# Kernel optimization log

Hardware: AMD Instinct MI355X
Metric: run time of the kernel (lower is better)

Reference implementation:

```python
import jax, jax.numpy as jnp
import numpy as np

N, E, G = 50000, 800000, 256
F_IN, H, C = 128, 64, 10
BN_EPS = 1e-5
N_CONV = 3


def _bn(x, g, b):
    # training-mode BatchNorm1d: biased batch statistics over dim 0
    m = jnp.mean(x, axis=0)
    v = jnp.mean((x - m) ** 2, axis=0)
    return g * (x - m) * jax.lax.rsqrt(v + BN_EPS) + b


def setup_inputs() -> dict:
    key = jax.random.key(0)
    ks = jax.random.split(key, 16)
    w = lambda k, s: jax.random.normal(k, s, jnp.float32) * 0.1
    inp = {
        "x": jax.random.normal(ks[0], (N, F_IN), jnp.float32),
        "edge_index": jax.random.randint(ks[1], (2, E), 0, N, jnp.int32),
        "batch": jnp.sort(jax.random.randint(ks[2], (N,), 0, G, jnp.int32)),
        # bn_feat
        "bn_feat_g": jnp.ones((F_IN,), jnp.float32),
        "bn_feat_b": jnp.full((F_IN,), 1e-4, jnp.float32),
        # conv_feat: GCNConv(gfn=True) == plain Linear
        "w_feat": w(ks[3], (F_IN, H)),
        "b_feat": jnp.zeros((H,), jnp.float32),
        # 3 GIN layers, params stacked on leading axis
        "gin_w1": w(ks[4], (N_CONV, H, H)),
        "gin_b1": jnp.zeros((N_CONV, H), jnp.float32),
        "gin_bn_g": jnp.ones((N_CONV, H), jnp.float32),
        "gin_bn_b": jnp.full((N_CONV, H), 1e-4, jnp.float32),
        "gin_w2": w(ks[5], (N_CONV, H, H)),
        "gin_b2": jnp.zeros((N_CONV, H), jnp.float32),
        # FC head: one bn+linear (num_fc_layers=2), bn_hidden, lin_class
        "bn_fc_g": jnp.ones((H,), jnp.float32),
        "bn_fc_b": jnp.full((H,), 1e-4, jnp.float32),
        "lin_w": w(ks[6], (H, H)),
        "lin_b": jnp.zeros((H,), jnp.float32),
        "bn_h_g": jnp.ones((H,), jnp.float32),
        "bn_h_b": jnp.full((H,), 1e-4, jnp.float32),
        "cls_w": w(ks[7], (H, C)),
        "cls_b": jnp.zeros((C,), jnp.float32),
    }
    return inp


def reference(x, edge_index, batch, bn_feat_g, bn_feat_b, w_feat, b_feat,
              gin_w1, gin_b1, gin_bn_g, gin_bn_b, gin_w2, gin_b2,
              bn_fc_g, bn_fc_b, lin_w, lin_b, bn_h_g, bn_h_b, cls_w, cls_b):
    src, dst = edge_index[0], edge_index[1]
    h = _bn(x, bn_feat_g, bn_feat_b)
    h = jax.nn.relu(h @ w_feat + b_feat)  # GCNConv(gfn=True): linear only
    for i in range(N_CONV):
        # GIN: (1+eps)*x + sum_{j in N(i)} x_j, eps = 0
        agg = jax.ops.segment_sum(h[src], dst, num_segments=N)
        z = h + agg
        z = jax.nn.relu(_bn(z @ gin_w1[i] + gin_b1[i], gin_bn_g[i], gin_bn_b[i]))
        h = jax.nn.relu(z @ gin_w2[i] + gin_b2[i])
    hg = jax.ops.segment_sum(h, batch, num_segments=G)  # global_add_pool
    hg = jax.nn.relu(_bn(hg, bn_fc_g, bn_fc_b) @ lin_w + lin_b)
    hg = _bn(hg, bn_h_g, bn_h_b)
    return hg @ cls_w + cls_b  # [G, C]
```

## Files before the change

kernel.cpp:

```cpp
#include <hip/hip_runtime.h>
#include <hip/hip_bf16.h>

#define NN 50000
#define EE 800000
#define GG 256
#define FF 128
#define HH 64
#define CC 10
#define BN_EPS 1e-5f
#define NB_SCAN ((NN + 255) / 256)

__device__ __forceinline__ float lane_bcast(float v, int srcLane) {
    union { float f; int i; } u; u.f = v;
    u.i = __builtin_amdgcn_readlane(u.i, srcLane);
    return u.f;
}

__global__ __launch_bounds__(256) void colstats128(const float* __restrict__ x,
                                                   float* __restrict__ sums, int n) {
    const int ROWS = (NN + 255) >> 8;
    int col = threadIdx.x & 127;
    int rh  = threadIdx.x >> 7;
    int r0  = blockIdx.x * ROWS;
    int r1  = min(n, r0 + ROWS);
    float s = 0.f, sq = 0.f;
    for (int r = r0 + rh; r < r1; r += 2) {
        float v = x[(size_t)r * FF + col];
        s += v; sq += v * v;
    }
    __shared__ float ls[256], lq[256];
    ls[threadIdx.x] = s; lq[threadIdx.x] = sq;
    __syncthreads();
    if (threadIdx.x < 128) {
        atomicAdd(&sums[col], ls[threadIdx.x] + ls[threadIdx.x + 128]);
        atomicAdd(&sums[128 + col], lq[threadIdx.x] + lq[threadIdx.x + 128]);
    }
}

__global__ void fold_feat(const float* __restrict__ sums, const float* __restrict__ g,
                          const float* __restrict__ b, const float* __restrict__ W,
                          const float* __restrict__ bias_in, float* __restrict__ Wf,
                          float* __restrict__ bf, float invn) {
    __shared__ float a[FF], c[FF];
    int j = threadIdx.x;
    float m = sums[j] * invn;
    float v = sums[FF + j] * invn - m * m;
    float aj = g[j] * rsqrtf(v + BN_EPS);
    a[j] = aj;
    c[j] = fmaf(-aj, m, b[j]);
    __syncthreads();
    for (int idx = j; idx < FF * HH; idx += FF) {
        int jj = idx >> 6;
        Wf[idx] = a[jj] * W[idx];
    }
    if (j < HH) {
        float acc = bias_in[j];
        for (int jj = 0; jj < FF; jj++) acc = fmaf(c[jj], W[jj * HH + j], acc);
        bf[j] = acc;
    }
}

__global__ __launch_bounds__(256) void gemm_feat(const float* __restrict__ x,
                                                 const float* __restrict__ Wf,
                                                 const float* __restrict__ bf,
                                                 float* __restrict__ h, int n) {
    int lane = threadIdx.x & 63;
    int wid  = threadIdx.x >> 6;
    float w[FF];
#pragma unroll
    for (int j = 0; j < FF; j++) w[j] = Wf[j * HH + lane];
    float bv = bf[lane];
    int wstride = gridDim.x * 4;
    for (int r = blockIdx.x * 4 + wid; r < n; r += wstride) {
        float xa = x[(size_t)r * FF + lane];
        float xb = x[(size_t)r * FF + 64 + lane];
        float a0 = bv, a1 = 0.f, a2 = 0.f, a3 = 0.f;
#pragma unroll
        for (int j = 0; j < 64; j += 4) {
            a0 = fmaf(lane_bcast(xa, j),     w[j],     a0);
            a1 = fmaf(lane_bcast(xa, j + 1), w[j + 1], a1);
            a2 = fmaf(lane_bcast(xa, j + 2), w[j + 2], a2);
            a3 = fmaf(lane_bcast(xa, j + 3), w[j + 3], a3);
        }
#pragma unroll
        for (int j = 0; j < 64; j += 4) {
            a0 = fmaf(lane_bcast(xb, j),     w[64 + j],     a0);
            a1 = fmaf(lane_bcast(xb, j + 1), w[64 + j + 1], a1);
            a2 = fmaf(lane_bcast(xb, j + 2), w[64 + j + 2], a2);
            a3 = fmaf(lane_bcast(xb, j + 3), w[64 + j + 3], a3);
        }
        h[(size_t)r * HH + lane] = fmaxf((a0 + a1) + (a2 + a3), 0.f);
    }
}

__global__ void hist_kernel(const int* __restrict__ dst, int* __restrict__ cnt, int e) {
    int i = blockIdx.x * blockDim.x + threadIdx.x;
    if (i < e) atomicAdd(&cnt[dst[i]], 1);
}

__global__ __launch_bounds__(256) void tile_sums(const int* __restrict__ cnt,
                                                 int* __restrict__ bsum, int n) {
    __shared__ int red[256];
    int i = blockIdx.x * 256 + threadIdx.x;
    red[threadIdx.x] = (i < n) ? cnt[i] : 0;
    __syncthreads();
    for (int off = 128; off > 0; off >>= 1) {
        if (threadIdx.x < off) red[threadIdx.x] += red[threadIdx.x + off];
        __syncthreads();
    }
    if (threadIdx.x == 0) bsum[blockIdx.x] = red[0];
}

__global__ __launch_bounds__(256) void scan_bsums(int* __restrict__ bsum, int nb) {
    __shared__ int s[256];
    int t = threadIdx.x;
    int v = (t < nb) ? bsum[t] : 0;
    s[t] = v;
    __syncthreads();
    for (int off = 1; off < 256; off <<= 1) {
        int x = (t >= off) ? s[t - off] : 0;
        __syncthreads();
        s[t] += x;
        __syncthreads();
    }
    if (t < nb) bsum[t] = s[t] - v;
}

__global__ __launch_bounds__(256) void scan_tiles_write(const int* __restrict__ cnt,
                                                        const int* __restrict__ bscan,
                                                        int* __restrict__ rowptr, int n) {
    __shared__ int s[256];
    int b = blockIdx.x, t = threadIdx.x;
    int i = b * 256 + t;
    int v = (i < n) ? cnt[i] : 0;
    s[t] = v;
    __syncthreads();
    for (int off = 1; off < 256; off <<= 1) {
        int x = (t >= off) ? s[t - off] : 0;
        __syncthreads();
        s[t] += x;
        __syncthreads();
    }
    if (i < n) rowptr[i] = bscan[b] + s[t] - v;
    if (b == 0 && t == 0) rowptr[n] = EE;
}

__global__ void fill_csr(const int* __restrict__ src, const int* __restrict__ dst,
                         const int* __restrict__ rowptr, int* __restrict__ cursor,
                         int* __restrict__ csr, int e) {
    int i = blockIdx.x * blockDim.x + threadIdx.x;
    if (i < e) {
        int d = dst[i];
        int slot = rowptr[d] + atomicAdd(&cursor[d], 1);
        csr[slot] = src[i];
    }
}

__global__ __launch_bounds__(256) void aggregate(const float* __restrict__ hin,
                                                 const int* __restrict__ rowptr,
                                                 const int* __restrict__ csr,
                                                 float* __restrict__ z, int n) {
    int lane  = threadIdx.x & 63;
    int wid   = threadIdx.x >> 6;
    int qcol  = (lane & 15) << 2;
    int eslot = lane >> 4;
    int wstride = gridDim.x * 4;
    for (int node = blockIdx.x * 4 + wid; node < n; node += wstride) {
        int lo = rowptr[node], hi = rowptr[node + 1];
        float ax = 0.f, ay = 0.f, az = 0.f, aw = 0.f;
        int base = lo;
        for (; base + 8 <= hi; base += 8) {
            int s0 = csr[base + eslot];
            int s1 = csr[base + 4 + eslot];
            const float4 v0 = *reinterpret_cast<const float4*>(&hin[(size_t)s0 * HH + qcol]);
            const float4 v1 = *reinterpret_cast<const float4*>(&hin[(size_t)s1 * HH + qcol]);
            ax += v0.x + v1.x; ay += v0.y + v1.y;
            az += v0.z + v1.z; aw += v0.w + v1.w;
        }
        if (base + 4 <= hi) {
            int s0 = csr[base + eslot];
            const float4 v0 = *reinterpret_cast<const float4*>(&hin[(size_t)s0 * HH + qcol]);
            ax += v0.x; ay += v0.y; az += v0.z; aw += v0.w;
            base += 4;
        }
        int rem = hi - base;
        if (eslot < rem) {
            int s0 = csr[base + eslot];
            const float4 v0 = *reinterpret_cast<const float4*>(&hin[(size_t)s0 * HH + qcol]);
            ax += v0.x; ay += v0.y; az += v0.z; aw += v0.w;
        }
        ax += __shfl_xor(ax, 16); ay += __shfl_xor(ay, 16);
        az += __shfl_xor(az, 16); aw += __shfl_xor(aw, 16);
        ax += __shfl_xor(ax, 32); ay += __shfl_xor(ay, 32);
        az += __shfl_xor(az, 32); aw += __shfl_xor(aw, 32);
        if (eslot == 0) {
            const float4 self = *reinterpret_cast<const float4*>(&hin[(size_t)node * HH + qcol]);
            float4 o;
            o.x = ax + self.x; o.y = ay + self.y;
            o.z = az + self.z; o.w = aw + self.w;
            *reinterpret_cast<float4*>(&z[(size_t)node * HH + qcol]) = o;
        }
    }
}

__global__ __launch_bounds__(256) void gin_lin1(float* __restrict__ zy,
                                                const float* __restrict__ W,
                                                const float* __restrict__ bias,
                                                float* __restrict__ stats, int n) {
    int lane = threadIdx.x & 63;
    int wid  = threadIdx.x >> 6;
    float w[HH];
#pragma unroll
    for (int j = 0; j < HH; j++) w[j] = W[j * HH + lane];
    float bv = bias[lane];
    float s = 0.f, sq = 0.f;
    int wstride = gridDim.x * 4;
    for (int r = blockIdx.x * 4 + wid; r < n; r += wstride) {
        float zv = zy[(size_t)r * HH + lane];
        float a0 = bv, a1 = 0.f;
#pragma unroll
        for (int j = 0; j < HH; j += 2) {
            a0 = fmaf(lane_bcast(zv, j),     w[j],     a0);
            a1 = fmaf(lane_bcast(zv, j + 1), w[j + 1], a1);
        }
        float acc = a0 + a1;
        zy[(size_t)r * HH + lane] = acc;
        s += acc; sq += acc * acc;
    }
    atomicAdd(&stats[lane], s);
    atomicAdd(&stats[HH + lane], sq);
}

__global__ void bn_params(const float* __restrict__ stats, const float* __restrict__ g,
                          const float* __restrict__ b, float* __restrict__ ac,
                          float invn, int cols) {
    int k = threadIdx.x;
    if (k < cols) {
        float m = stats[k] * invn;
        float v = stats[cols + k] * invn - m * m;
        float a = g[k] * rsqrtf(v + BN_EPS);
        ac[k] = a;
        ac[cols + k] = fmaf(-a, m, b[k]);
    }
}

__global__ __launch_bounds__(256) void gin_lin2(float* __restrict__ yh,
                                                const float* __restrict__ ac,
                                                const float* __restrict__ W2,
                                                const float* __restrict__ b2, int n) {
    int lane = threadIdx.x & 63;
    int wid  = threadIdx.x >> 6;
    float w[HH];
#pragma unroll
    for (int j = 0; j < HH; j++) w[j] = W2[j * HH + lane];
    float a = ac[lane], c = ac[HH + lane];
    float bv = b2[lane];
    int wstride = gridDim.x * 4;
    for (int r = blockIdx.x * 4 + wid; r < n; r += wstride) {
        float yv = yh[(size_t)r * HH + lane];
        float zv = fmaxf(fmaf(a, yv, c), 0.f);
        float a0 = bv, a1 = 0.f;
#pragma unroll
        for (int j = 0; j < HH; j += 2) {
            a0 = fmaf(lane_bcast(zv, j),     w[j],     a0);
            a1 = fmaf(lane_bcast(zv, j + 1), w[j + 1], a1);
        }
        yh[(size_t)r * HH + lane] = fmaxf(a0 + a1, 0.f);
    }
}

__global__ __launch_bounds__(64) void pool_kernel(const float* __restrict__ h,
                                                  const int* __restrict__ batch,
                                                  float* __restrict__ hg, int n) {
    int g = blockIdx.x;
    int lo = 0, hi = n;
    while (lo < hi) { int mid = (lo + hi) >> 1; if (batch[mid] < g) lo = mid + 1; else hi = mid; }
    int start = lo;
    lo = start; hi = n;
    while (lo < hi) { int mid = (lo + hi) >> 1; if (batch[mid] < g + 1) lo = mid + 1; else hi = mid; }
    int end = lo;
    int lane = threadIdx.x;
    float acc = 0.f;
    for (int r = start; r < end; r++) acc += h[(size_t)r * HH + lane];
    hg[g * HH + lane] = acc;
}

__global__ __launch_bounds__(256) void head1(const float* __restrict__ hg,
                                             const float* __restrict__ g,
                                             const float* __restrict__ b,
                                             const float* __restrict__ lw,
                                             const float* __restrict__ lb,
                                             float* __restrict__ hh) {
    __shared__ float Wt[HH * HH];
    __shared__ float s1[256], s2[256];
    __shared__ float aa[HH], cc[HH];
    int t = threadIdx.x;
    for (int i = t; i < HH * HH; i += 256) {
        int j = i >> 6, k = i & 63;
        Wt[k * HH + j] = lw[i];
    }
    int col = t & 63, q = t >> 6;
    float s = 0.f, sq = 0.f;
    for (int r = q; r < GG; r += 4) { float v = hg[r * HH + col]; s += v; sq += v * v; }
    s1[t] = s; s2[t] = sq;
    __syncthreads();
    if (t < HH) {
        float S = s1[t] + s1[t + 64] + s1[t + 128] + s1[t + 192];
        float Q = s2[t] + s2[t + 64] + s2[t + 128] + s2[t + 192];
        float m = S * (1.f / GG), v = Q * (1.f / GG) - m * m;
        float a = g[t] * rsqrtf(v + BN_EPS);
        aa[t] = a; cc[t] = fmaf(-a, m, b[t]);
    }
    __syncthreads();
    float rv[HH];
#pragma unroll
    for (int j = 0; j < HH; j++) rv[j] = fmaf(aa[j], hg[t * HH + j], cc[j]);
#pragma unroll 4
    for (int k = 0; k < HH; k++) {
        float acc = lb[k];
#pragma unroll
        for (int j = 0; j < HH; j++) acc = fmaf(rv[j], Wt[k * HH + j], acc);
        hh[t * HH + k] = fmaxf(acc, 0.f);
    }
}

__global__ __launch_bounds__(256) void head2(const float* __restrict__ hh,
                                             const float* __restrict__ g,
                                             const float* __restrict__ b,
                                             const float* __restrict__ cw,
                                             const float* __restrict__ cb,
                                             float* __restrict__ out) {
    __shared__ float s1[256], s2[256];
    __shared__ float aa[HH], cc[HH];
    __shared__ float Wc[HH * CC];
    __shared__ float cbs[CC];
    int t = threadIdx.x;
    for (int i = t; i < HH * CC; i += 256) Wc[i] = cw[i];
    if (t < CC) cbs[t] = cb[t];
    int col = t & 63, q = t >> 6;
    float s = 0.f, sq = 0.f;
    for (int r = q; r < GG; r += 4) { float v = hh[r * HH + col]; s += v; sq += v * v; }
    s1[t] = s; s2[t] = sq;
    __syncthreads();
    if (t < HH) {
        float S = s1[t] + s1[t + 64] + s1[t + 128] + s1[t + 192];
        float Q = s2[t] + s2[t + 64] + s2[t + 128] + s2[t + 192];
        float m = S * (1.f / GG), v = Q * (1.f / GG) - m * m;
        float a = g[t] * rsqrtf(v + BN_EPS);
        aa[t] = a; cc[t] = fmaf(-a, m, b[t]);
    }
    __syncthreads();
    float acc[CC];
#pragma unroll
    for (int c2 = 0; c2 < CC; c2++) acc[c2] = cbs[c2];
#pragma unroll
    for (int j = 0; j < HH; j++) {
        float v = fmaf(aa[j], hh[t * HH + j], cc[j]);
#pragma unroll
        for (int c2 = 0; c2 < CC; c2++) acc[c2] = fmaf(v, Wc[j * CC + c2], acc[c2]);
    }
#pragma unroll
    for (int c2 = 0; c2 < CC; c2++) out[t * CC + c2] = acc[c2];
}

extern "C" void kernel_launch(void* const* d_in, const int* in_sizes, int n_in,
                              void* d_out, int out_size, void* d_ws, size_t ws_size,
                              hipStream_t stream) {
    const float* x        = (const float*)d_in[0];
    const int*   ei       = (const int*)d_in[1];
    const int*   srcp     = ei;
    const int*   dstp     = ei + EE;
    const int*   batchp   = (const int*)d_in[2];
    const float* bnf_g    = (const float*)d_in[3];
    const float* bnf_b    = (const float*)d_in[4];
    const float* w_feat   = (const float*)d_in[5];
    const float* b_feat   = (const float*)d_in[6];
    const float* gin_w1   = (const float*)d_in[7];
    const float* gin_b1   = (const float*)d_in[8];
    const float* gin_bn_g = (const float*)d_in[9];
    const float* gin_bn_b = (const float*)d_in[10];
    const float* gin_w2   = (const float*)d_in[11];
    const float* gin_b2   = (const float*)d_in[12];
    const float* bn_fc_g  = (const float*)d_in[13];
    const float* bn_fc_b  = (const float*)d_in[14];
    const float* lin_w    = (const float*)d_in[15];
    const float* lin_b    = (const float*)d_in[16];
    const float* bn_h_g   = (const float*)d_in[17];
    const float* bn_h_b   = (const float*)d_in[18];
    const float* cls_w    = (const float*)d_in[19];
    const float* cls_b    = (const float*)d_in[20];
    float* out = (float*)d_out;

    float* ws   = (float*)d_ws;
    float* bufA = ws;
    float* bufB = bufA + (size_t)NN * HH;
    float* Wf   = bufB + (size_t)NN * HH;
    float* bff  = Wf + FF * HH;
    float* stats= bff + HH;
    float* ac   = stats + 2 * FF;
    float* hh   = ac + 2 * HH;
    float* hg   = hh + GG * HH;
    int* rowptr = (int*)(hg + GG * HH);
    int* cnt    = rowptr + (NN + 1);
    int* bsum   = cnt + NN;
    int* csr    = bsum + NB_SCAN;

    hipMemsetAsync(stats, 0, 2 * FF * sizeof(float), stream);
    colstats128<<<256, 256, 0, stream>>>(x, stats, NN);
    fold_feat<<<1, 128, 0, stream>>>(stats, bnf_g, bnf_b, w_feat, b_feat, Wf, bff, 1.0f / NN);
    gemm_feat<<<512, 256, 0, stream>>>(x, Wf, bff, bufA, NN);

    hipMemsetAsync(cnt, 0, NN * sizeof(int), stream);
    hist_kernel<<<(EE + 255) / 256, 256, 0, stream>>>(dstp, cnt, EE);
    tile_sums<<<NB_SCAN, 256, 0, stream>>>(cnt, bsum, NN);
    scan_bsums<<<1, 256, 0, stream>>>(bsum, NB_SCAN);
    scan_tiles_write<<<NB_SCAN, 256, 0, stream>>>(cnt, bsum, rowptr, NN);
    hipMemsetAsync(cnt, 0, NN * sizeof(int), stream);
    fill_csr<<<(EE + 255) / 256, 256, 0, stream>>>(srcp, dstp, rowptr, cnt, csr, EE);

    float* hin = bufA;
    float* hout = bufB;
    for (int i = 0; i < 3; i++) {
        aggregate<<<2048, 256, 0, stream>>>(hin, rowptr, csr, hout, NN);
        hipMemsetAsync(stats, 0, 2 * HH * sizeof(float), stream);
        gin_lin1<<<512, 256, 0, stream>>>(hout, gin_w1 + i * HH * HH, gin_b1 + i * HH, stats, NN);
        bn_params<<<1, 64, 0, stream>>>(stats, gin_bn_g + i * HH, gin_bn_b + i * HH, ac, 1.0f / NN, HH);
        gin_lin2<<<512, 256, 0, stream>>>(hout, ac, gin_w2 + i * HH * HH, gin_b2 + i * HH, NN);
        float* tmp = hin; hin = hout; hout = tmp;
    }

    pool_kernel<<<GG, 64, 0, stream>>>(hin, batchp, hg, NN);
    head1<<<1, 256, 0, stream>>>(hg, bn_fc_g, bn_fc_b, lin_w, lin_b, hh);
    head2<<<1, 256, 0, stream>>>(hh, bn_h_g, bn_h_b, cls_w, cls_b, out);
}
```

Baseline: 733.3 us.

## Stage GIN linear rows in shared memory tiles and widen pooling blocks

The GIN linear kernels now load 64-row tiles into shared memory with float4 loads and read the row operand from LDS as float4 broadcasts, replacing the per-element readlane broadcasts. BN-apply+ReLU is applied during the staging load in gin_lin2. One block per tile is launched, which also brings __syncthreads overhead and extra LDS traffic. Pooling uses 256 threads per graph with a shared-memory reduction instead of one 64-thread serial loop.

```diff
diff --git a/kernel.cpp b/kernel.cpp
--- a/kernel.cpp
+++ b/kernel.cpp
@@ -9,6 +9,8 @@
 #define CC 10
 #define BN_EPS 1e-5f
 #define NB_SCAN ((NN + 255) / 256)
+#define TROWS 64
+#define NTILES ((NN + TROWS - 1) / TROWS)
 
 __device__ __forceinline__ float lane_bcast(float v, int srcLane) {
     union { float f; int i; } u; u.f = v;
@@ -207,6 +209,7 @@
                                                 const float* __restrict__ W,
                                                 const float* __restrict__ bias,
                                                 float* __restrict__ stats, int n) {
+    __shared__ float zt[TROWS][HH];
     int lane = threadIdx.x & 63;
     int wid  = threadIdx.x >> 6;
     float w[HH];
@@ -214,18 +217,34 @@
     for (int j = 0; j < HH; j++) w[j] = W[j * HH + lane];
     float bv = bias[lane];
     float s = 0.f, sq = 0.f;
-    int wstride = gridDim.x * 4;
-    for (int r = blockIdx.x * 4 + wid; r < n; r += wstride) {
-        float zv = zy[(size_t)r * HH + lane];
-        float a0 = bv, a1 = 0.f;
-#pragma unroll
-        for (int j = 0; j < HH; j += 2) {
-            a0 = fmaf(lane_bcast(zv, j),     w[j],     a0);
-            a1 = fmaf(lane_bcast(zv, j + 1), w[j + 1], a1);
-        }
-        float acc = a0 + a1;
-        zy[(size_t)r * HH + lane] = acc;
-        s += acc; sq += acc * acc;
+    for (int tile = blockIdx.x; tile < NTILES; tile += gridDim.x) {
+        int rbase = tile * TROWS;
+        __syncthreads();
+#pragma unroll
+        for (int stp = 0; stp < 4; stp++) {
+            int idx = stp * 1024 + threadIdx.x * 4;
+            int rr = idx >> 6, cc = idx & 63;
+            int row = rbase + rr;
+            float4 v = (row < n) ? *reinterpret_cast<const float4*>(&zy[(size_t)row * HH + cc])
+                                 : make_float4(0.f, 0.f, 0.f, 0.f);
+            *reinterpret_cast<float4*>(&zt[rr][cc]) = v;
+        }
+        __syncthreads();
+        int rr_end = min(wid * 16 + 16, n - rbase);
+        for (int rr = wid * 16; rr < rr_end; rr++) {
+            float a0 = bv, a1 = 0.f, a2 = 0.f, a3 = 0.f;
+#pragma unroll
+            for (int jq = 0; jq < 16; jq++) {
+                float4 zq = *reinterpret_cast<const float4*>(&zt[rr][jq * 4]);
+                a0 = fmaf(zq.x, w[jq * 4 + 0], a0);
+                a1 = fmaf(zq.y, w[jq * 4 + 1], a1);
+                a2 = fmaf(zq.z, w[jq * 4 + 2], a2);
+                a3 = fmaf(zq.w, w[jq * 4 + 3], a3);
+            }
+            float acc = (a0 + a1) + (a2 + a3);
+            zy[(size_t)(rbase + rr) * HH + lane] = acc;
+            s += acc; sq += acc * acc;
+        }
     }
     atomicAdd(&stats[lane], s);
     atomicAdd(&stats[HH + lane], sq);
@@ -248,30 +267,52 @@
                                                 const float* __restrict__ ac,
                                                 const float* __restrict__ W2,
                                                 const float* __restrict__ b2, int n) {
+    __shared__ float zt[TROWS][HH];
     int lane = threadIdx.x & 63;
     int wid  = threadIdx.x >> 6;
     float w[HH];
 #pragma unroll
     for (int j = 0; j < HH; j++) w[j] = W2[j * HH + lane];
-    float a = ac[lane], c = ac[HH + lane];
     float bv = b2[lane];
-    int wstride = gridDim.x * 4;
-    for (int r = blockIdx.x * 4 + wid; r < n; r += wstride) {
-        float yv = yh[(size_t)r * HH + lane];
-        float zv = fmaxf(fmaf(a, yv, c), 0.f);
-        float a0 = bv, a1 = 0.f;
-#pragma unroll
-        for (int j = 0; j < HH; j += 2) {
-            a0 = fmaf(lane_bcast(zv, j),     w[j],     a0);
-            a1 = fmaf(lane_bcast(zv, j + 1), w[j + 1], a1);
-        }
-        yh[(size_t)r * HH + lane] = fmaxf(a0 + a1, 0.f);
-    }
-}
-
-__global__ __launch_bounds__(64) void pool_kernel(const float* __restrict__ h,
-                                                  const int* __restrict__ batch,
-                                                  float* __restrict__ hg, int n) {
+    int cc0 = (threadIdx.x * 4) & 63;
+    float4 aq = *reinterpret_cast<const float4*>(&ac[cc0]);
+    float4 cq = *reinterpret_cast<const float4*>(&ac[HH + cc0]);
+    for (int tile = blockIdx.x; tile < NTILES; tile += gridDim.x) {
+        int rbase = tile * TROWS;
+        __syncthreads();
+#pragma unroll
+        for (int stp = 0; stp < 4; stp++) {
+            int idx = stp * 1024 + threadIdx.x * 4;
+            int rr = idx >> 6, cc = idx & 63;
+            int row = rbase + rr;
+            float4 v = (row < n) ? *reinterpret_cast<const float4*>(&yh[(size_t)row * HH + cc])
+                                 : make_float4(0.f, 0.f, 0.f, 0.f);
+            v.x = fmaxf(fmaf(aq.x, v.x, cq.x), 0.f);
+            v.y = fmaxf(fmaf(aq.y, v.y, cq.y), 0.f);
+            v.z = fmaxf(fmaf(aq.z, v.z, cq.z), 0.f);
+            v.w = fmaxf(fmaf(aq.w, v.w, cq.w), 0.f);
+            *reinterpret_cast<float4*>(&zt[rr][cc]) = v;
+        }
+        __syncthreads();
+        int rr_end = min(wid * 16 + 16, n - rbase);
+        for (int rr = wid * 16; rr < rr_end; rr++) {
+            float a0 = bv, a1 = 0.f, a2 = 0.f, a3 = 0.f;
+#pragma unroll
+            for (int jq = 0; jq < 16; jq++) {
+                float4 zq = *reinterpret_cast<const float4*>(&zt[rr][jq * 4]);
+                a0 = fmaf(zq.x, w[jq * 4 + 0], a0);
+                a1 = fmaf(zq.y, w[jq * 4 + 1], a1);
+                a2 = fmaf(zq.z, w[jq * 4 + 2], a2);
+                a3 = fmaf(zq.w, w[jq * 4 + 3], a3);
+            }
+            yh[(size_t)(rbase + rr) * HH + lane] = fmaxf((a0 + a1) + (a2 + a3), 0.f);
+        }
+    }
+}
+
+__global__ __launch_bounds__(256) void pool_kernel(const float* __restrict__ h,
+                                                   const int* __restrict__ batch,
+                                                   float* __restrict__ hg, int n) {
     int g = blockIdx.x;
     int lo = 0, hi = n;
     while (lo < hi) { int mid = (lo + hi) >> 1; if (batch[mid] < g) lo = mid + 1; else hi = mid; }
@@ -279,10 +320,16 @@
     lo = start; hi = n;
     while (lo < hi) { int mid = (lo + hi) >> 1; if (batch[mid] < g + 1) lo = mid + 1; else hi = mid; }
     int end = lo;
-    int lane = threadIdx.x;
+    int lane = threadIdx.x & 63;
+    int q    = threadIdx.x >> 6;
     float acc = 0.f;
-    for (int r = start; r < end; r++) acc += h[(size_t)r * HH + lane];
-    hg[g * HH + lane] = acc;
+    for (int r = start + q; r < end; r += 4) acc += h[(size_t)r * HH + lane];
+    __shared__ float red[256];
+    red[threadIdx.x] = acc;
+    __syncthreads();
+    if (threadIdx.x < HH)
+        hg[g * HH + threadIdx.x] = red[threadIdx.x] + red[threadIdx.x + 64] +
+                                   red[threadIdx.x + 128] + red[threadIdx.x + 192];
 }
 
 __global__ __launch_bounds__(256) void head1(const float* __restrict__ hg,
@@ -423,13 +470,13 @@
     for (int i = 0; i < 3; i++) {
         aggregate<<<2048, 256, 0, stream>>>(hin, rowptr, csr, hout, NN);
         hipMemsetAsync(stats, 0, 2 * HH * sizeof(float), stream);
-        gin_lin1<<<512, 256, 0, stream>>>(hout, gin_w1 + i * HH * HH, gin_b1 + i * HH, stats, NN);
+        gin_lin1<<<NTILES, 256, 0, stream>>>(hout, gin_w1 + i * HH * HH, gin_b1 + i * HH, stats, NN);
         bn_params<<<1, 64, 0, stream>>>(stats, gin_bn_g + i * HH, gin_bn_b + i * HH, ac, 1.0f / NN, HH);
-        gin_lin2<<<512, 256, 0, stream>>>(hout, ac, gin_w2 + i * HH * HH, gin_b2 + i * HH, NN);
+        gin_lin2<<<NTILES, 256, 0, stream>>>(hout, ac, gin_w2 + i * HH * HH, gin_b2 + i * HH, NN);
         float* tmp = hin; hin = hout; hout = tmp;
     }
 
-    pool_kernel<<<GG, 64, 0, stream>>>(hin, batchp, hg, NN);
+    pool_kernel<<<GG, 256, 0, stream>>>(hin, batchp, hg, NN);
     head1<<<1, 256, 0, stream>>>(hg, bn_fc_g, bn_fc_b, lin_w, lin_b, hh);
     head2<<<1, 256, 0, stream>>>(hh, bn_h_g, bn_h_b, cls_w, cls_b, out);
 }
```

New measurement: 771.4 us. +5.2%, slower.
